# Performance work log

Hardware: AMD Instinct MI355X
Metric: run time of the kernel (lower is better)

The kernel has to match this reference:

```python
import math
import jax, jax.numpy as jnp
import numpy as np

N_FFT = 1024
HOP = 320
WIN = 800
SR = 32000
N_MELS = 128
FMIN = 0.0
FMAX = SR / 2.0
NUM_BINS = N_FFT // 2 + 1  # 513
PREEMPH = 0.97


def _hann_window(n):
    # torch.hann_window(n, periodic=False): 0.5 - 0.5*cos(2*pi*i/(n-1))
    i = np.arange(n, dtype=np.float64)
    return (0.5 - 0.5 * np.cos(2.0 * np.pi * i / (n - 1))).astype(np.float32)


def _fourier_basis():
    offset = (N_FFT - WIN) // 2
    win_full = np.zeros(N_FFT, dtype=np.float64)
    win_full[offset:offset + WIN] = _hann_window(WIN)
    n = np.arange(N_FFT, dtype=np.float64)[None, :]
    k = np.arange(NUM_BINS, dtype=np.float64)[:, None]
    ang = 2.0 * np.pi * k * (n / float(N_FFT))
    cos_k = np.cos(ang) * win_full
    sin_k = -np.sin(ang) * win_full
    return np.concatenate([cos_k, sin_k], axis=0).astype(np.float32)  # [2*513, 1024]


def _kaldi_mel_banks():
    # torchaudio.compliance.kaldi.get_mel_banks with vtln_warp_factor=1.0
    num_fft_bins = N_FFT // 2
    fft_bin_width = SR / float(N_FFT)
    mel = lambda f: 1127.0 * np.log(1.0 + f / 700.0)
    mel_low, mel_high = mel(FMIN), mel(FMAX)
    delta = (mel_high - mel_low) / (N_MELS + 1)
    left = mel_low + np.arange(N_MELS, dtype=np.float64) * delta  # [M]
    right = left + 2.0 * delta
    freqs = fft_bin_width * np.arange(num_fft_bins, dtype=np.float64)
    m = mel(freqs)[None, :]  # [1, 512]
    up = (m - left[:, None]) / delta
    down = (right[:, None] - m) / delta
    bank = np.maximum(0.0, np.minimum(up, down))  # [128, 512]
    bank = np.pad(bank, ((0, 0), (0, 1)))  # pad one zero column -> [128, 513]
    return bank.astype(np.float32)


def setup_inputs() -> dict:
    key = jax.random.key(0)
    x = jax.random.normal(key, (32, 320000), dtype=jnp.float32)
    return {
        "x": x,
        "fourier_basis": jnp.asarray(_fourier_basis()),
        "mel_basis": jnp.asarray(_kaldi_mel_banks()),
    }


def reference(x, fourier_basis, mel_basis):
    # preemphasis: conv1d with kernel [-0.97, 1.0] (cross-correlation)
    y = x[:, 1:] - PREEMPH * x[:, :-1]  # [B, T-1]
    # center pad by n_fft//2
    pad = N_FFT // 2
    y = jnp.pad(y, ((0, 0), (pad, pad)))
    Tp = y.shape[1]
    frames = (Tp - N_FFT) // HOP + 1
    # frame extraction: [B, frames, n_fft]
    idx = jnp.arange(frames)[:, None] * HOP + jnp.arange(N_FFT)[None, :]
    f = y[:, idx]
    # explicit DFT via dense matmul: [B, 2*num_bins, frames]
    spec = jnp.einsum('btn,cn->bct', f, fourier_basis)
    real = spec[:, :NUM_BINS, :]
    imag = spec[:, NUM_BINS:, :]
    power = real * real + imag * imag  # [B, num_bins, frames]
    mel = jnp.einsum('mf,bft->bmt', mel_basis, power)
    log_mel = (jnp.log(mel + 1e-05) + 4.5) / 5.0
    return log_mel
```

## Files before the change

### kernel.cpp

```cpp
#include <hip/hip_runtime.h>
#include <math.h>

typedef _Float16 half8 __attribute__((ext_vector_type(8)));
typedef float f32x4 __attribute__((ext_vector_type(4)));

constexpr int kNFFT    = 1024;
constexpr int kHop     = 320;
constexpr int kMels    = 128;
constexpr int kFrames  = 1000;
constexpr int kBatch   = 32;
constexpr int kXLen    = 320000;
constexpr int kYLen    = kXLen - 1;
constexpr int kYPad    = 328704;
constexpr int kYOff    = 512;
constexpr float kPre   = 0.97f;
constexpr int kPStride = 544;

constexpr size_t kYLvl     = (size_t)kBatch * kYPad;
constexpr size_t kFragLvl  = 64ull * 32 * 64 * 8;
constexpr size_t kFragOff  = 2 * kYLvl;
constexpr size_t kMelFrOff = kFragOff + 2 * kFragLvl;
constexpr size_t kMelFrSz  = 8ull * 17 * 64 * 8;
constexpr size_t kPowOff   = kMelFrOff + kMelFrSz;

__global__ void prep_y(const float* __restrict__ x, _Float16* __restrict__ yp) {
    int i = blockIdx.x * 256 + threadIdx.x;
    int e0 = i * 8;
    if (e0 >= kYPad) return;
    int b = blockIdx.y;
    const float* xb = x + (size_t)b * kXLen;
    int yi = e0 - kYOff;
    float v[8];
    if (yi >= 0 && yi <= kXLen - 9) {
        float4 A = *(const float4*)(xb + yi);
        float4 B = *(const float4*)(xb + yi + 4);
        float C = xb[yi + 8];
        v[0] = A.y - kPre * A.x;  v[1] = A.z - kPre * A.y;
        v[2] = A.w - kPre * A.z;  v[3] = B.x - kPre * A.w;
        v[4] = B.y - kPre * B.x;  v[5] = B.z - kPre * B.y;
        v[6] = B.w - kPre * B.z;  v[7] = C   - kPre * B.w;
    } else {
        #pragma unroll
        for (int j = 0; j < 8; ++j) {
            int g = yi + j;
            v[j] = (g >= 0 && g < kYLen) ? xb[g + 1] - kPre * xb[g] : 0.0f;
        }
    }
    half8 hv, mv;
    #pragma unroll
    for (int j = 0; j < 8; ++j) {
        _Float16 h = (_Float16)v[j];
        hv[j] = h;
        mv[j] = (_Float16)(v[j] - (float)h);
    }
    size_t idx = (size_t)b * kYPad + e0;
    *(half8*)(yp + idx) = hv;
    *(half8*)(yp + idx + kYLvl) = mv;
}

__global__ void prep_frags(const float* __restrict__ basis, _Float16* __restrict__ fr) {
    int id = blockIdx.x * 256 + threadIdx.x;
    int L  = id & 63;
    int ks = (id >> 6) & 31;
    int g  = id >> 11;
    int r  = 16 * g + (L & 15);
    int orig = (r <= 512) ? r : r + 1;
    const float* src = basis + (size_t)orig * kNFFT + 32 * ks + (L >> 4) * 8;
    _Float16* dst = fr + (size_t)id * 8;
    #pragma unroll
    for (int j = 0; j < 8; ++j) {
        float a = src[j];
        _Float16 h = (_Float16)a;
        _Float16 m = (_Float16)(a - (float)h);
        dst[j] = h;
        dst[j + kFragLvl] = m;
    }
}

__global__ void prep_melfr(const float* __restrict__ melb, _Float16* __restrict__ fr) {
    int id = blockIdx.x * 256 + threadIdx.x;
    if (id >= 8 * 17 * 64) return;
    int f = id / 1088;
    int rem = id - f * 1088;
    int ks = rem >> 6;
    int L = rem & 63;
    int m = 16 * f + (L & 15);
    int kb = 32 * ks + (L >> 4) * 8;
    _Float16* dst = fr + (size_t)id * 8;
    #pragma unroll
    for (int j = 0; j < 8; ++j) {
        int k = kb + j;
        dst[j] = (k < 513) ? (_Float16)melb[(size_t)m * 513 + k] : (_Float16)0.0f;
    }
}

__global__ __launch_bounds__(512, 4)
void stft_power(const _Float16* __restrict__ frags,
                const _Float16* __restrict__ ypad,
                _Float16* __restrict__ pw) {
    __shared__ __align__(16) _Float16 ash[2][16 * 512];
    const int tid  = threadIdx.x;
    const int w    = tid >> 6;
    const int lane = tid & 63;
    const int quad = lane >> 4;
    const int l16  = lane & 15;
    const int nt = blockIdx.x, g = blockIdx.y, b = blockIdx.z;
    const int t0 = nt * 256 + w * 32;
    const _Float16* yb0 = ypad + (size_t)b * kYPad;
    const _Float16* yb1 = yb0 + kYLvl;

    f32x4 acc[8][2] = {};

    auto stageA = [&](int ks, int pbuf) {
        #pragma unroll
        for (int c = 0; c < 2; ++c) {
            int slot = w + 8 * c;
            int f = slot & 7, lv = slot >> 3;
            int Gf = (f < 4) ? (4 * g + f) : (32 + 4 * g + (f - 4));
            const _Float16* gp = frags + (size_t)lv * kFragLvl
                               + ((size_t)(Gf * 32 + ks) * 64 + lane) * 8;
            __builtin_amdgcn_global_load_lds(
                (const __attribute__((address_space(1))) void*)gp,
                (__attribute__((address_space(3))) void*)&ash[pbuf][slot * 512],
                16, 0, 0);
        }
    };
    auto loadB = [&](int ks, half8* bh, half8* bm) {
        #pragma unroll
        for (int nf = 0; nf < 2; ++nf) {
            int off = (t0 + nf * 16 + l16) * kHop + ks * 32 + quad * 8;
            bh[nf] = *(const half8*)(yb0 + off);
            bm[nf] = *(const half8*)(yb1 + off);
        }
    };
    auto compute = [&](int pbuf, half8* bh, half8* bm) {
        #pragma unroll
        for (int f = 0; f < 8; ++f) {
            half8 afh = *(const half8*)&ash[pbuf][f * 512 + lane * 8];
            half8 afm = *(const half8*)&ash[pbuf][(8 + f) * 512 + lane * 8];
            #pragma unroll
            for (int nf = 0; nf < 2; ++nf) {
                f32x4 a = acc[f][nf];
                a = __builtin_amdgcn_mfma_f32_16x16x32_f16(afh, bh[nf], a, 0, 0, 0);
                a = __builtin_amdgcn_mfma_f32_16x16x32_f16(afm, bh[nf], a, 0, 0, 0);
                a = __builtin_amdgcn_mfma_f32_16x16x32_f16(afh, bm[nf], a, 0, 0, 0);
                acc[f][nf] = a;
            }
        }
    };

    half8 bhA[2], bmA[2], bhB[2], bmB[2];
    stageA(0, 0);
    loadB(0, bhA, bmA);
    for (int kss = 0; kss < 16; ++kss) {
        int ks = 2 * kss;
        __syncthreads();
        stageA(ks + 1, 1);
        loadB(ks + 1, bhB, bmB);
        compute(0, bhA, bmA);
        __syncthreads();
        if (ks + 2 < 32) {
            stageA(ks + 2, 0);
            loadB(ks + 2, bhA, bmA);
        }
        compute(1, bhB, bmB);
    }

    #pragma unroll
    for (int mf = 0; mf < 4; ++mf) {
        int b0 = 64 * g + 16 * mf + 4 * quad;
        #pragma unroll
        for (int nf = 0; nf < 2; ++nf) {
            int t = t0 + nf * 16 + l16;
            size_t row = ((size_t)((b << 10) + t)) * kPStride;
            struct alignas(8) h4 { _Float16 v[4]; } pp;
            #pragma unroll
            for (int r = 0; r < 4; ++r) {
                float pA = acc[mf][nf][r];
                float pB = acc[4 + mf][nf][r];
                float p2 = pA * pA + pB * pB;
                if (g == 0 && mf == 0 && quad == 0 && r == 0) {
                    p2 = pA * pA;
                    pw[row + 512] = (_Float16)(pB * pB);
                }
                pp.v[r] = (_Float16)p2;
            }
            *(decltype(pp)*)&pw[row + b0] = pp;
        }
    }
}

__global__ __launch_bounds__(256)
void mel_mfma(const _Float16* __restrict__ melfr, const _Float16* __restrict__ pw,
              float* __restrict__ out) {
    const int tid  = threadIdx.x;
    const int w    = tid >> 6;
    const int lane = tid & 63;
    const int quad = lane >> 4;
    const int l16  = lane & 15;
    const int nt = blockIdx.x, b = blockIdx.y;
    const int t = nt * 64 + w * 16 + l16;

    f32x4 acc[8] = {};
    const _Float16* prow = pw + ((size_t)((b << 10) + t)) * kPStride;
    for (int ks = 0; ks < 17; ++ks) {
        half8 bp = *(const half8*)(prow + 32 * ks + quad * 8);
        #pragma unroll
        for (int f = 0; f < 8; ++f) {
            half8 af = *(const half8*)(melfr + ((size_t)(f * 17 + ks) * 64 + lane) * 8);
            acc[f] = __builtin_amdgcn_mfma_f32_16x16x32_f16(af, bp, acc[f], 0, 0, 0);
        }
    }
    if (t < kFrames) {
        #pragma unroll
        for (int f = 0; f < 8; ++f) {
            #pragma unroll
            for (int r = 0; r < 4; ++r) {
                int m = 16 * f + 4 * quad + r;
                out[((size_t)(b * kMels + m)) * kFrames + t] =
                    (__logf(acc[f][r] + 1e-5f) + 4.5f) * 0.2f;
            }
        }
    }
}

extern "C" void kernel_launch(void* const* d_in, const int* in_sizes, int n_in,
                              void* d_out, int out_size, void* d_ws, size_t ws_size,
                              hipStream_t stream) {
    const float* x     = (const float*)d_in[0];
    const float* basis = (const float*)d_in[1];
    const float* melb  = (const float*)d_in[2];
    float* out = (float*)d_out;

    _Float16* ws    = (_Float16*)d_ws;
    _Float16* ypad  = ws;
    _Float16* frags = ws + kFragOff;
    _Float16* melfr = ws + kMelFrOff;
    _Float16* pw    = ws + kPowOff;

    prep_y<<<dim3(kYPad / 8 / 256 + 1, kBatch), 256, 0, stream>>>(x, ypad);
    prep_frags<<<dim3(131072 / 256), 256, 0, stream>>>(basis, frags);
    prep_melfr<<<dim3((8 * 17 * 64 + 255) / 256), 256, 0, stream>>>(melb, melfr);
    stft_power<<<dim3(4, 8, kBatch), 512, 0, stream>>>(frags, ypad, pw);
    mel_mfma<<<dim3(16, kBatch), 256, 0, stream>>>(melfr, pw, out);
}
```

Baseline: 296.5 us.

## Switch STFT matmul to 32x32x16 MFMA and merge prep kernels into one launch

The STFT power kernel now uses 32x32x16 f16 MFMA tiles instead of 16x16x32, with the Fourier basis fragments re-laid out to match and the B operand loaded as 32 frames by 16 k. This raises work per MFMA instruction and per LDS read, and halves the number of B register loads per frame tile. Separately, the three preprocessing kernels are fused into one launch with block-range dispatch, removing two kernel launches. The epilogue is rewritten to map the 32x32 accumulator layout back to power bins, which adds some risk in the index mapping.

```diff
diff --git a/kernel.cpp b/kernel.cpp
--- a/kernel.cpp
+++ b/kernel.cpp
@@ -3,6 +3,7 @@
 
 typedef _Float16 half8 __attribute__((ext_vector_type(8)));
 typedef float f32x4 __attribute__((ext_vector_type(4)));
+typedef float f32x16 __attribute__((ext_vector_type(16)));
 
 constexpr int kNFFT    = 1024;
 constexpr int kHop     = 320;
@@ -17,80 +18,91 @@
 constexpr int kPStride = 544;
 
 constexpr size_t kYLvl     = (size_t)kBatch * kYPad;
-constexpr size_t kFragLvl  = 64ull * 32 * 64 * 8;
+constexpr size_t kFragLvl  = 32ull * 64 * 64 * 8;
 constexpr size_t kFragOff  = 2 * kYLvl;
 constexpr size_t kMelFrOff = kFragOff + 2 * kFragLvl;
 constexpr size_t kMelFrSz  = 8ull * 17 * 64 * 8;
 constexpr size_t kPowOff   = kMelFrOff + kMelFrSz;
 
-__global__ void prep_y(const float* __restrict__ x, _Float16* __restrict__ yp) {
-    int i = blockIdx.x * 256 + threadIdx.x;
-    int e0 = i * 8;
-    if (e0 >= kYPad) return;
-    int b = blockIdx.y;
-    const float* xb = x + (size_t)b * kXLen;
-    int yi = e0 - kYOff;
-    float v[8];
-    if (yi >= 0 && yi <= kXLen - 9) {
-        float4 A = *(const float4*)(xb + yi);
-        float4 B = *(const float4*)(xb + yi + 4);
-        float C = xb[yi + 8];
-        v[0] = A.y - kPre * A.x;  v[1] = A.z - kPre * A.y;
-        v[2] = A.w - kPre * A.z;  v[3] = B.x - kPre * A.w;
-        v[4] = B.y - kPre * B.x;  v[5] = B.z - kPre * B.y;
-        v[6] = B.w - kPre * B.z;  v[7] = C   - kPre * B.w;
+constexpr int kYJobBlks   = (kYPad / 8 + 255) / 256;
+constexpr int kYJobTotal  = kYJobBlks * kBatch;
+constexpr int kFragBlks   = 131072 / 256;
+constexpr int kMelBlks    = (8 * 17 * 64) / 256;
+constexpr int kPrepGrid   = kYJobTotal + kFragBlks + kMelBlks;
+
+__global__ void prep_all(const float* __restrict__ x, const float* __restrict__ basis,
+                         const float* __restrict__ melb, _Float16* __restrict__ ws) {
+    _Float16* ypad  = ws;
+    _Float16* fr    = ws + kFragOff;
+    _Float16* melfr = ws + kMelFrOff;
+    const int bid = blockIdx.x;
+    const int tid = threadIdx.x;
+
+    if (bid < kYJobTotal) {
+        int b = bid / kYJobBlks;
+        int blk = bid - b * kYJobBlks;
+        int e0 = (blk * 256 + tid) * 8;
+        if (e0 >= kYPad) return;
+        const float* xb = x + (size_t)b * kXLen;
+        int yi = e0 - kYOff;
+        float v[8];
+        if (yi >= 0 && yi <= kXLen - 9) {
+            float4 A = *(const float4*)(xb + yi);
+            float4 B = *(const float4*)(xb + yi + 4);
+            float C = xb[yi + 8];
+            v[0] = A.y - kPre * A.x;  v[1] = A.z - kPre * A.y;
+            v[2] = A.w - kPre * A.z;  v[3] = B.x - kPre * A.w;
+            v[4] = B.y - kPre * B.x;  v[5] = B.z - kPre * B.y;
+            v[6] = B.w - kPre * B.z;  v[7] = C   - kPre * B.w;
+        } else {
+            #pragma unroll
+            for (int j = 0; j < 8; ++j) {
+                int g = yi + j;
+                v[j] = (g >= 0 && g < kYLen) ? xb[g + 1] - kPre * xb[g] : 0.0f;
+            }
+        }
+        half8 hv, mv;
+        #pragma unroll
+        for (int j = 0; j < 8; ++j) {
+            _Float16 h = (_Float16)v[j];
+            hv[j] = h;
+            mv[j] = (_Float16)(v[j] - (float)h);
+        }
+        size_t idx = (size_t)b * kYPad + e0;
+        *(half8*)(ypad + idx) = hv;
+        *(half8*)(ypad + idx + kYLvl) = mv;
+    } else if (bid < kYJobTotal + kFragBlks) {
+        int id = (bid - kYJobTotal) * 256 + tid;
+        int L  = id & 63;
+        int kh = (id >> 6) & 63;
+        int G  = id >> 12;
+        int r  = 32 * G + (L & 31);
+        int orig = (r <= 512) ? r : r + 1;
+        const float* src = basis + (size_t)orig * kNFFT + 16 * kh + (L >> 5) * 8;
+        _Float16* dst = fr + (size_t)id * 8;
+        #pragma unroll
+        for (int j = 0; j < 8; ++j) {
+            float a = src[j];
+            _Float16 h = (_Float16)a;
+            _Float16 m = (_Float16)(a - (float)h);
+            dst[j] = h;
+            dst[j + kFragLvl] = m;
+        }
     } else {
+        int id = (bid - kYJobTotal - kFragBlks) * 256 + tid;
+        if (id >= 8 * 17 * 64) return;
+        int f = id / 1088;
+        int rem = id - f * 1088;
+        int ks = rem >> 6;
+        int L = rem & 63;
+        int m = 16 * f + (L & 15);
+        int kb = 32 * ks + (L >> 4) * 8;
+        _Float16* dst = melfr + (size_t)id * 8;
         #pragma unroll
         for (int j = 0; j < 8; ++j) {
-            int g = yi + j;
-            v[j] = (g >= 0 && g < kYLen) ? xb[g + 1] - kPre * xb[g] : 0.0f;
-        }
-    }
-    half8 hv, mv;
-    #pragma unroll
-    for (int j = 0; j < 8; ++j) {
-        _Float16 h = (_Float16)v[j];
-        hv[j] = h;
-        mv[j] = (_Float16)(v[j] - (float)h);
-    }
-    size_t idx = (size_t)b * kYPad + e0;
-    *(half8*)(yp + idx) = hv;
-    *(half8*)(yp + idx + kYLvl) = mv;
-}
-
-__global__ void prep_frags(const float* __restrict__ basis, _Float16* __restrict__ fr) {
-    int id = blockIdx.x * 256 + threadIdx.x;
-    int L  = id & 63;
-    int ks = (id >> 6) & 31;
-    int g  = id >> 11;
-    int r  = 16 * g + (L & 15);
-    int orig = (r <= 512) ? r : r + 1;
-    const float* src = basis + (size_t)orig * kNFFT + 32 * ks + (L >> 4) * 8;
-    _Float16* dst = fr + (size_t)id * 8;
-    #pragma unroll
-    for (int j = 0; j < 8; ++j) {
-        float a = src[j];
-        _Float16 h = (_Float16)a;
-        _Float16 m = (_Float16)(a - (float)h);
-        dst[j] = h;
-        dst[j + kFragLvl] = m;
-    }
-}
-
-__global__ void prep_melfr(const float* __restrict__ melb, _Float16* __restrict__ fr) {
-    int id = blockIdx.x * 256 + threadIdx.x;
-    if (id >= 8 * 17 * 64) return;
-    int f = id / 1088;
-    int rem = id - f * 1088;
-    int ks = rem >> 6;
-    int L = rem & 63;
-    int m = 16 * f + (L & 15);
-    int kb = 32 * ks + (L >> 4) * 8;
-    _Float16* dst = fr + (size_t)id * 8;
-    #pragma unroll
-    for (int j = 0; j < 8; ++j) {
-        int k = kb + j;
-        dst[j] = (k < 513) ? (_Float16)melb[(size_t)m * 513 + k] : (_Float16)0.0f;
+            int k = kb + j;
+            dst[j] = (k < 513) ? (_Float16)melb[(size_t)m * 513 + k] : (_Float16)0.0f;
+        }
     }
 }
 
@@ -102,23 +114,24 @@
     const int tid  = threadIdx.x;
     const int w    = tid >> 6;
     const int lane = tid & 63;
-    const int quad = lane >> 4;
-    const int l16  = lane & 15;
+    const int hi   = lane >> 5;
+    const int l32  = lane & 31;
     const int nt = blockIdx.x, g = blockIdx.y, b = blockIdx.z;
     const int t0 = nt * 256 + w * 32;
     const _Float16* yb0 = ypad + (size_t)b * kYPad;
     const _Float16* yb1 = yb0 + kYLvl;
 
-    f32x4 acc[8][2] = {};
+    f32x16 acc[4] = {};
 
     auto stageA = [&](int ks, int pbuf) {
         #pragma unroll
         for (int c = 0; c < 2; ++c) {
             int slot = w + 8 * c;
-            int f = slot & 7, lv = slot >> 3;
-            int Gf = (f < 4) ? (4 * g + f) : (32 + 4 * g + (f - 4));
+            int lv = slot >> 3, kh2 = (slot >> 2) & 1, mf = slot & 3;
+            int G = (mf < 2) ? (2 * g + mf) : (16 + 2 * g + (mf - 2));
+            int kh = 2 * ks + kh2;
             const _Float16* gp = frags + (size_t)lv * kFragLvl
-                               + ((size_t)(Gf * 32 + ks) * 64 + lane) * 8;
+                               + ((size_t)(G * 64 + kh) * 64 + lane) * 8;
             __builtin_amdgcn_global_load_lds(
                 (const __attribute__((address_space(1))) void*)gp,
                 (__attribute__((address_space(3))) void*)&ash[pbuf][slot * 512],
@@ -127,24 +140,24 @@
     };
     auto loadB = [&](int ks, half8* bh, half8* bm) {
         #pragma unroll
-        for (int nf = 0; nf < 2; ++nf) {
-            int off = (t0 + nf * 16 + l16) * kHop + ks * 32 + quad * 8;
-            bh[nf] = *(const half8*)(yb0 + off);
-            bm[nf] = *(const half8*)(yb1 + off);
+        for (int kh2 = 0; kh2 < 2; ++kh2) {
+            int off = (t0 + l32) * kHop + 16 * (2 * ks + kh2) + hi * 8;
+            bh[kh2] = *(const half8*)(yb0 + off);
+            bm[kh2] = *(const half8*)(yb1 + off);
         }
     };
     auto compute = [&](int pbuf, half8* bh, half8* bm) {
         #pragma unroll
-        for (int f = 0; f < 8; ++f) {
-            half8 afh = *(const half8*)&ash[pbuf][f * 512 + lane * 8];
-            half8 afm = *(const half8*)&ash[pbuf][(8 + f) * 512 + lane * 8];
-            #pragma unroll
-            for (int nf = 0; nf < 2; ++nf) {
-                f32x4 a = acc[f][nf];
-                a = __builtin_amdgcn_mfma_f32_16x16x32_f16(afh, bh[nf], a, 0, 0, 0);
-                a = __builtin_amdgcn_mfma_f32_16x16x32_f16(afm, bh[nf], a, 0, 0, 0);
-                a = __builtin_amdgcn_mfma_f32_16x16x32_f16(afh, bm[nf], a, 0, 0, 0);
-                acc[f][nf] = a;
+        for (int kh2 = 0; kh2 < 2; ++kh2) {
+            #pragma unroll
+            for (int mf = 0; mf < 4; ++mf) {
+                half8 afh = *(const half8*)&ash[pbuf][(kh2 * 4 + mf) * 512 + lane * 8];
+                half8 afm = *(const half8*)&ash[pbuf][(8 + kh2 * 4 + mf) * 512 + lane * 8];
+                f32x16 a = acc[mf];
+                a = __builtin_amdgcn_mfma_f32_32x32x16_f16(afh, bh[kh2], a, 0, 0, 0);
+                a = __builtin_amdgcn_mfma_f32_32x32x16_f16(afm, bh[kh2], a, 0, 0, 0);
+                a = __builtin_amdgcn_mfma_f32_32x32x16_f16(afh, bm[kh2], a, 0, 0, 0);
+                acc[mf] = a;
             }
         }
     };
@@ -166,26 +179,27 @@
         compute(1, bhB, bmB);
     }
 
+    const int t = t0 + l32;
+    const size_t row = ((size_t)((b << 10) + t)) * kPStride;
     #pragma unroll
-    for (int mf = 0; mf < 4; ++mf) {
-        int b0 = 64 * g + 16 * mf + 4 * quad;
-        #pragma unroll
-        for (int nf = 0; nf < 2; ++nf) {
-            int t = t0 + nf * 16 + l16;
-            size_t row = ((size_t)((b << 10) + t)) * kPStride;
+    for (int mf = 0; mf < 2; ++mf) {
+        #pragma unroll
+        for (int q = 0; q < 4; ++q) {
+            int binbase = 64 * g + 32 * mf + 8 * q + 4 * hi;
             struct alignas(8) h4 { _Float16 v[4]; } pp;
             #pragma unroll
-            for (int r = 0; r < 4; ++r) {
-                float pA = acc[mf][nf][r];
-                float pB = acc[4 + mf][nf][r];
+            for (int r2 = 0; r2 < 4; ++r2) {
+                int r = 4 * q + r2;
+                float pA = acc[mf][r];
+                float pB = acc[mf + 2][r];
                 float p2 = pA * pA + pB * pB;
-                if (g == 0 && mf == 0 && quad == 0 && r == 0) {
+                if (g == 0 && mf == 0 && q == 0 && hi == 0 && r2 == 0) {
                     p2 = pA * pA;
                     pw[row + 512] = (_Float16)(pB * pB);
                 }
-                pp.v[r] = (_Float16)p2;
-            }
-            *(decltype(pp)*)&pw[row + b0] = pp;
+                pp.v[r2] = (_Float16)p2;
+            }
+            *(decltype(pp)*)&pw[row + binbase] = pp;
         }
     }
 }
@@ -233,14 +247,11 @@
     float* out = (float*)d_out;
 
     _Float16* ws    = (_Float16*)d_ws;
-    _Float16* ypad  = ws;
     _Float16* frags = ws + kFragOff;
     _Float16* melfr = ws + kMelFrOff;
     _Float16* pw    = ws + kPowOff;
 
-    prep_y<<<dim3(kYPad / 8 / 256 + 1, kBatch), 256, 0, stream>>>(x, ypad);
-    prep_frags<<<dim3(131072 / 256), 256, 0, stream>>>(basis, frags);
-    prep_melfr<<<dim3((8 * 17 * 64 + 255) / 256), 256, 0, stream>>>(melb, melfr);
-    stft_power<<<dim3(4, 8, kBatch), 512, 0, stream>>>(frags, ypad, pw);
+    prep_all<<<dim3(kPrepGrid), 256, 0, stream>>>(x, basis, melb, ws);
+    stft_power<<<dim3(4, 8, kBatch), 512, 0, stream>>>(frags, ws, pw);
     mel_mfma<<<dim3(16, kBatch), 256, 0, stream>>>(melfr, pw, out);
 }
```

After: 323.7 us. 1.09x slower.
